# Performance work log

Hardware: AMD Instinct MI355X
Metric: run time of the kernel (lower is better)

Reference implementation:

```python
import jax, jax.numpy as jnp
import numpy as np

B, NB, K, C, CM, POS = 8, 1024, 9, 32, 128, 2
SIGMA = 0.5
NEG_SLOPE = 0.01  # nn.LeakyReLU default
BN_EPS = 1e-5


def _leaky(x):
    return jnp.where(x >= 0, x, NEG_SLOPE * x)


def _batchnorm(x, gamma, beta):
    # BatchNorm1d, training-mode batch statistics over the point dimension
    mu = jnp.mean(x, axis=0)
    var = jnp.mean((x - mu) ** 2, axis=0)
    return gamma * (x - mu) * jax.lax.rsqrt(var + BN_EPS) + beta


def setup_inputs() -> dict:
    key = jax.random.key(0)
    ks = jax.random.split(key, 8)
    N = B * NB
    positions = jax.random.normal(ks[0], (N, POS), jnp.float32)
    weights = jax.random.normal(ks[1], (N, C), jnp.float32)
    batch = jnp.full((B,), NB, dtype=jnp.int32)  # uniform point counts per graph
    # KernelConv params: kernel_init='grid' -> 3x3 grid of offsets spanning +-sigma
    g = jnp.linspace(-SIGMA, SIGMA, 3, dtype=jnp.float32)
    kernel_positions = jnp.stack(jnp.meshgrid(g, g, indexing='ij'), axis=-1).reshape(K, POS)
    kernel_weights = (jax.random.normal(ks[2], (K, C, C), jnp.float32) / np.float32(np.sqrt(C * K)))
    conv_norm_gamma = jnp.ones((C,), jnp.float32)
    conv_norm_beta = jnp.zeros((C,), jnp.float32)
    # PyG MLP([C, CM, C+POS], act_first=True, plain_last=True)
    W1 = jax.random.normal(ks[3], (C, CM), jnp.float32) / np.float32(np.sqrt(C))
    b1 = jnp.zeros((CM,), jnp.float32)
    bn_gamma = jnp.ones((CM,), jnp.float32)
    bn_beta = jnp.zeros((CM,), jnp.float32)
    W2 = jax.random.normal(ks[4], (CM, C + POS), jnp.float32) / np.float32(np.sqrt(CM))
    b2 = jnp.zeros((C + POS,), jnp.float32)
    return dict(positions=positions, weights=weights, batch=batch,
                kernel_positions=kernel_positions, kernel_weights=kernel_weights,
                conv_norm_gamma=conv_norm_gamma, conv_norm_beta=conv_norm_beta,
                W1=W1, b1=b1, bn_gamma=bn_gamma, bn_beta=bn_beta, W2=W2, b2=b2)


def reference(positions, weights, batch, kernel_positions, kernel_weights,
              conv_norm_gamma, conv_norm_beta, W1, b1, bn_gamma, bn_beta, W2, b2):
    N = positions.shape[0]
    # --- KernelConv: each point spawns K components at pos + kernel offset ---
    conv_pos = (positions[:, None, :] + kernel_positions[None, :, :])  # [N,K,2]
    conv_w = jnp.einsum('nc,kcd->nkd', weights, kernel_weights)        # [N,K,C]
    conv_pos = conv_pos.reshape(B, NB * K, POS)
    conv_w = conv_w.reshape(B, NB * K, C)
    # --- KernelSample: evaluate Gaussian mixture at original positions ---
    p = positions.reshape(B, NB, POS)
    d2 = (jnp.sum(p * p, -1)[:, :, None]
          + jnp.sum(conv_pos * conv_pos, -1)[:, None, :]
          - 2.0 * jnp.einsum('bnd,bmd->bnm', p, conv_pos))             # [B,NB,NB*K]
    Kmat = jnp.exp(-d2 / (2.0 * SIGMA * SIGMA))
    sampled = jnp.einsum('bnm,bmc->bnc', Kmat, conv_w).reshape(N, C)
    x = _leaky(sampled)                                                 # KernelSample nonlinearity
    # conv_norm + residual add of input weights
    x = _batchnorm(x, conv_norm_gamma, conv_norm_beta) + weights
    # MLP: lin -> act -> batchnorm (act_first) -> plain last lin
    h = _batchnorm(_leaky(x @ W1 + b1), bn_gamma, bn_beta)
    mlp_out = h @ W2 + b2                                               # [N, POS + C]
    delta_pos, delta_w = mlp_out[:, :POS], mlp_out[:, POS:]
    return positions + delta_pos, x + delta_w
```

## Files before the change

kernel.cpp:

```cpp
#include <hip/hip_runtime.h>
#include <hip/hip_bf16.h>

#define BB    8
#define NBB   1024
#define KK    9
#define CC    32
#define CMM   128
#define NTOT  (BB*NBB)
#define MM    (NBB*KK)
#define NEG   0.01f
#define EPS   1e-5f
#define SQL2  1.6986436f

#define OFF_CWT   0
#define SZ_CWT    (BB*CC*MM/2)
#define OFF_QPX   (OFF_CWT + SZ_CWT)
#define OFF_QPY   (OFF_QPX + BB*MM)
#define OFF_X0    (OFF_QPY + BB*MM)
#define OFF_X     (OFF_X0 + NTOT*CC)
#define OFF_H0    (OFF_X + NTOT*CC)
#define OFF_ST    (OFF_H0 + NTOT*CMM)

typedef __attribute__((ext_vector_type(8))) short short8;
typedef __attribute__((ext_vector_type(4))) float f32x4;
typedef __attribute__((ext_vector_type(2))) float f32x2;

static __device__ __forceinline__ unsigned short f2bf_rne(float f) {
    __hip_bfloat16 h = __float2bfloat16(f);
    return *reinterpret_cast<unsigned short*>(&h);
}

__global__ __launch_bounds__(256) void k_convw(const float* __restrict__ pos,
                                               const float* __restrict__ kpos,
                                               const float* __restrict__ w,
                                               const float* __restrict__ kw,
                                               float* __restrict__ qpx,
                                               float* __restrict__ qpy,
                                               float* __restrict__ stats,
                                               short* __restrict__ cwT) {
    __shared__ unsigned short kwl[KK*CC*CC];
    __shared__ unsigned short tile[2*32*144];
    int t = threadIdx.x;
    int l = t & 63, wv = t >> 6;
    int lane15 = l & 15, quad = l >> 4;
    int blk = blockIdx.x;
    int b = blk & 7, nbl = blk >> 3;

    if (blk == 0 && t < 320) stats[t] = 0.f;
    #pragma unroll
    for (int rep = 0; rep < 2; ++rep) {
        int gid = rep*65536 + blk*256 + t;
        if (gid < BB*MM) {
            int bb = gid / MM;
            int m = gid - bb*MM;
            int np = m / 9, k9 = m - np*9;
            float qx = pos[((size_t)(bb*NBB + np))*2 + 0] + kpos[k9*2 + 0];
            float qy = pos[((size_t)(bb*NBB + np))*2 + 1] + kpos[k9*2 + 1];
            qpx[gid] = SQL2*qx;
            qpy[gid] = SQL2*qy;
        }
    }
    for (int u = t; u < KK*CC*CC/4; u += 256) {
        int flat = u*4;
        int row = flat >> 5;
        int c0 = flat & 31;
        int kk = row >> 5, cp = row & 31;
        f32x4 v = *(const f32x4*)&kw[flat];
        kwl[(kk*CC + c0+0)*CC + cp] = f2bf_rne(v.x);
        kwl[(kk*CC + c0+1)*CC + cp] = f2bf_rne(v.y);
        kwl[(kk*CC + c0+2)*CC + cp] = f2bf_rne(v.z);
        kwl[(kk*CC + c0+3)*CC + cp] = f2bf_rne(v.w);
    }
    int n = b*NBB + nbl*32 + (wv & 1)*16 + lane15;
    f32x4 w0 = *(const f32x4*)&w[(size_t)n*CC + quad*8];
    f32x4 w1 = *(const f32x4*)&w[(size_t)n*CC + quad*8 + 4];
    union { unsigned short us[8]; short8 s; } bfr;
    bfr.us[0] = f2bf_rne(w0.x); bfr.us[1] = f2bf_rne(w0.y);
    bfr.us[2] = f2bf_rne(w0.z); bfr.us[3] = f2bf_rne(w0.w);
    bfr.us[4] = f2bf_rne(w1.x); bfr.us[5] = f2bf_rne(w1.y);
    bfr.us[6] = f2bf_rne(w1.z); bfr.us[7] = f2bf_rne(w1.w);
    __syncthreads();
    if (wv < 2) {
        f32x4 acc[KK][2];
        #pragma unroll
        for (int kk = 0; kk < KK; ++kk)
            #pragma unroll
            for (int ct = 0; ct < 2; ++ct) {
                int c = ct*16 + lane15;
                short8 afr = *(const short8*)&kwl[(kk*CC + c)*CC + quad*8];
                acc[kk][ct] = __builtin_amdgcn_mfma_f32_16x16x32_bf16(
                    afr, bfr.s, (f32x4)0.f, 0, 0, 0);
            }
        unsigned short* tw = tile + wv*4608;
        #pragma unroll
        for (int kk = 0; kk < KK; ++kk)
            #pragma unroll
            for (int ct = 0; ct < 2; ++ct)
                #pragma unroll
                for (int reg = 0; reg < 4; ++reg) {
                    int c = ct*16 + quad*4 + reg;
                    tw[c*144 + lane15*9 + kk] = f2bf_rne(acc[kk][ct][reg]);
                }
    }
    __syncthreads();
    short* dst = cwT + (size_t)b*CC*MM + (size_t)(nbl*32)*9;
    #pragma unroll
    for (int it = 0; it < 5; ++it) {
        int u = it*256 + t;
        if (u < 1152) {
            int c = u / 36, seg = u - c*36;
            const unsigned short* src = tile + (seg < 18 ? 0 : 4608)
                                      + c*144 + (seg < 18 ? seg : seg - 18)*8;
            short8 v = *(const short8*)src;
            *(short8*)&dst[(size_t)c*MM + seg*8] = v;
        }
    }
}

__global__ __launch_bounds__(1024) void k_sample(const float* __restrict__ pos,
                                                 const float* __restrict__ qpx,
                                                 const float* __restrict__ qpy,
                                                 const short* __restrict__ cwT,
                                                 float* __restrict__ x0,
                                                 float* __restrict__ s1) {
    __shared__ float red[16*32*36];
    __shared__ float sstat[64];
    int t = threadIdx.x;
    int l = t & 63, wv = t >> 6;
    int blk = blockIdx.x;
    int b = blk & 7, nblk = blk >> 3;
    int lane15 = l & 15, quad = l >> 4;
    int nbase = b*NBB + nblk*32;
    if (t < 64) sstat[t] = 0.f;

    float px[2], py[2];
    #pragma unroll
    for (int nt = 0; nt < 2; ++nt) {
        int n = nbase + nt*16 + lane15;
        px[nt] = SQL2*pos[(size_t)n*2];
        py[nt] = SQL2*pos[(size_t)n*2 + 1];
    }
    f32x4 acc[2][2];
    acc[0][0] = (f32x4)0.f; acc[0][1] = (f32x4)0.f;
    acc[1][0] = (f32x4)0.f; acc[1][1] = (f32x4)0.f;

    const float* qx = qpx + (size_t)b*MM;
    const float* qy = qpy + (size_t)b*MM;
    const short* ca0 = cwT + (size_t)b*CC*MM + (size_t)lane15*MM;
    const short* ca1 = ca0 + (size_t)16*MM;

    int m0 = wv*576 + quad*8;
    short8 a0 = *(const short8*)&ca0[m0];
    short8 a1 = *(const short8*)&ca1[m0];
    f32x4 X0 = *(const f32x4*)&qx[m0], X1 = *(const f32x4*)&qx[m0 + 4];
    f32x4 Y0 = *(const f32x4*)&qy[m0], Y1 = *(const f32x4*)&qy[m0 + 4];
    for (int kk = 0; kk < 18; ++kk) {
        int mn = m0 + (kk < 17 ? 32 : 0);
        short8 na0 = *(const short8*)&ca0[mn];
        short8 na1 = *(const short8*)&ca1[mn];
        f32x4 nX0 = *(const f32x4*)&qx[mn], nX1 = *(const f32x4*)&qx[mn + 4];
        f32x4 nY0 = *(const f32x4*)&qy[mn], nY1 = *(const f32x4*)&qy[mn + 4];
        #pragma unroll
        for (int nt = 0; nt < 2; ++nt) {
            f32x2 PX = {px[nt], px[nt]};
            f32x2 PY = {py[nt], py[nt]};
            f32x2 dx0 = (f32x2){X0.x, X0.y} - PX;
            f32x2 dy0 = (f32x2){Y0.x, Y0.y} - PY;
            f32x2 t0 = dx0*dx0; t0 = dy0*dy0 + t0;
            f32x2 dx1 = (f32x2){X0.z, X0.w} - PX;
            f32x2 dy1 = (f32x2){Y0.z, Y0.w} - PY;
            f32x2 t1 = dx1*dx1; t1 = dy1*dy1 + t1;
            f32x2 dx2 = (f32x2){X1.x, X1.y} - PX;
            f32x2 dy2 = (f32x2){Y1.x, Y1.y} - PY;
            f32x2 t2 = dx2*dx2; t2 = dy2*dy2 + t2;
            f32x2 dx3 = (f32x2){X1.z, X1.w} - PX;
            f32x2 dy3 = (f32x2){Y1.z, Y1.w} - PY;
            f32x2 t3 = dx3*dx3; t3 = dy3*dy3 + t3;
            float e0 = __builtin_amdgcn_exp2f(-t0.x);
            float e1 = __builtin_amdgcn_exp2f(-t0.y);
            float e2 = __builtin_amdgcn_exp2f(-t1.x);
            float e3 = __builtin_amdgcn_exp2f(-t1.y);
            float e4 = __builtin_amdgcn_exp2f(-t2.x);
            float e5 = __builtin_amdgcn_exp2f(-t2.y);
            float e6 = __builtin_amdgcn_exp2f(-t3.x);
            float e7 = __builtin_amdgcn_exp2f(-t3.y);
            union { unsigned int u[4]; short8 s; } bf;
            bf.u[0] = (__float_as_uint(e0) >> 16) | (__float_as_uint(e1) & 0xffff0000u);
            bf.u[1] = (__float_as_uint(e2) >> 16) | (__float_as_uint(e3) & 0xffff0000u);
            bf.u[2] = (__float_as_uint(e4) >> 16) | (__float_as_uint(e5) & 0xffff0000u);
            bf.u[3] = (__float_as_uint(e6) >> 16) | (__float_as_uint(e7) & 0xffff0000u);
            acc[nt][0] = __builtin_amdgcn_mfma_f32_16x16x32_bf16(a0, bf.s, acc[nt][0], 0, 0, 0);
            acc[nt][1] = __builtin_amdgcn_mfma_f32_16x16x32_bf16(a1, bf.s, acc[nt][1], 0, 0, 0);
        }
        a0 = na0; a1 = na1;
        X0 = nX0; X1 = nX1; Y0 = nY0; Y1 = nY1;
        m0 = mn;
    }
    #pragma unroll
    for (int nt = 0; nt < 2; ++nt)
        #pragma unroll
        for (int ct = 0; ct < 2; ++ct) {
            int n = nt*16 + lane15, c = ct*16 + quad*4;
            *(f32x4*)&red[(wv*32 + n)*36 + c] = acc[nt][ct];
        }
    __syncthreads();
    if (t < 256) {
        int nr = t >> 3, c0 = (t & 7)*4;
        f32x4 v = (f32x4)0.f;
        #pragma unroll
        for (int wp = 0; wp < 16; ++wp)
            v = v + *(const f32x4*)&red[(wp*32 + nr)*36 + c0];
        v.x = v.x >= 0.f ? v.x : NEG*v.x;
        v.y = v.y >= 0.f ? v.y : NEG*v.y;
        v.z = v.z >= 0.f ? v.z : NEG*v.z;
        v.w = v.w >= 0.f ? v.w : NEG*v.w;
        *(f32x4*)&x0[((size_t)(nbase + nr))*CC + c0] = v;
        float s0 = v.x, s1v = v.y, s2v = v.z, s3v = v.w;
        float q0 = v.x*v.x, q1 = v.y*v.y, q2 = v.z*v.z, q3 = v.w*v.w;
        #pragma unroll
        for (int mk = 8; mk <= 32; mk <<= 1) {
            s0 += __shfl_xor(s0, mk); s1v += __shfl_xor(s1v, mk);
            s2v += __shfl_xor(s2v, mk); s3v += __shfl_xor(s3v, mk);
            q0 += __shfl_xor(q0, mk); q1 += __shfl_xor(q1, mk);
            q2 += __shfl_xor(q2, mk); q3 += __shfl_xor(q3, mk);
        }
        if (l < 8) {
            atomicAdd(&sstat[c0 + 0], s0);  atomicAdd(&sstat[c0 + 1], s1v);
            atomicAdd(&sstat[c0 + 2], s2v); atomicAdd(&sstat[c0 + 3], s3v);
            atomicAdd(&sstat[32 + c0 + 0], q0); atomicAdd(&sstat[32 + c0 + 1], q1);
            atomicAdd(&sstat[32 + c0 + 2], q2); atomicAdd(&sstat[32 + c0 + 3], q3);
        }
    }
    __syncthreads();
    if (t < 64) atomicAdd(&s1[t], sstat[t]);
}

__global__ __launch_bounds__(256) void k_mlp1(const float* __restrict__ x0,
                                              const float* __restrict__ wts,
                                              const float* __restrict__ gma,
                                              const float* __restrict__ bta,
                                              const float* __restrict__ W1,
                                              const float* __restrict__ b1,
                                              const float* __restrict__ s1,
                                              float* __restrict__ x,
                                              float* __restrict__ h0,
                                              float* __restrict__ s2) {
    __shared__ float tile[32*68];
    int t = threadIdx.x;
    int l = t & 63, wv = t >> 6;
    int blk = blockIdx.x;
    int nb = blk >> 2, jq = blk & 3;
    int n = nb*64 + l;
    int j0 = jq*32 + wv*8;

    float xv[32];
    #pragma unroll
    for (int c = 0; c < 32; ++c) {
        float mu  = s1[c] * (1.f/NTOT);
        float var = s1[32+c]*(1.f/NTOT) - mu*mu;
        float a   = gma[c] * rsqrtf(var + EPS);
        float v   = x0[(size_t)n*CC + c];
        xv[c] = a*(v - mu) + bta[c] + wts[(size_t)n*CC + c];
    }
    if (jq == 0 && wv == 0) {
        #pragma unroll
        for (int c = 0; c < 32; c += 4)
            *(float4*)&x[(size_t)n*CC + c] = make_float4(xv[c], xv[c+1], xv[c+2], xv[c+3]);
    }
    float acc[8];
    *(f32x4*)&acc[0] = *(const f32x4*)&b1[j0];
    *(f32x4*)&acc[4] = *(const f32x4*)&b1[j0 + 4];
    #pragma unroll 8
    for (int c = 0; c < 32; ++c) {
        float xc = xv[c];
        const float* w1r = W1 + c*CMM + j0;
        f32x4 wa = *(const f32x4*)&w1r[0];
        f32x4 wb = *(const f32x4*)&w1r[4];
        acc[0] = fmaf(xc, wa.x, acc[0]); acc[1] = fmaf(xc, wa.y, acc[1]);
        acc[2] = fmaf(xc, wa.z, acc[2]); acc[3] = fmaf(xc, wa.w, acc[3]);
        acc[4] = fmaf(xc, wb.x, acc[4]); acc[5] = fmaf(xc, wb.y, acc[5]);
        acc[6] = fmaf(xc, wb.z, acc[6]); acc[7] = fmaf(xc, wb.w, acc[7]);
    }
    #pragma unroll
    for (int jj = 0; jj < 8; ++jj) {
        acc[jj] = acc[jj] >= 0.f ? acc[jj] : NEG*acc[jj];
        tile[(wv*8 + jj)*68 + l] = acc[jj];
    }
    float* hd = h0 + (size_t)n*CMM + j0;
    *(float4*)&hd[0] = make_float4(acc[0], acc[1], acc[2], acc[3]);
    *(float4*)&hd[4] = make_float4(acc[4], acc[5], acc[6], acc[7]);
    __syncthreads();
    if (t < 256) {
        int jl = t >> 3, grp = t & 7;
        float lsum = 0.f, lsq = 0.f;
        #pragma unroll
        for (int q = 0; q < 2; ++q) {
            f32x4 v = *(const f32x4*)&tile[jl*68 + grp*8 + q*4];
            lsum += v.x + v.y + v.z + v.w;
            lsq = fmaf(v.x, v.x, fmaf(v.y, v.y, fmaf(v.z, v.z, fmaf(v.w, v.w, lsq))));
        }
        lsum += __shfl_xor(lsum, 1); lsq += __shfl_xor(lsq, 1);
        lsum += __shfl_xor(lsum, 2); lsq += __shfl_xor(lsq, 2);
        lsum += __shfl_xor(lsum, 4); lsq += __shfl_xor(lsq, 4);
        if (grp == 0) {
            int jg = jq*32 + jl;
            atomicAdd(&s2[jg], lsum);
            atomicAdd(&s2[CMM + jg], lsq);
        }
    }
}

__global__ __launch_bounds__(256) void k_mlp2(const float* __restrict__ h0,
                                              const float* __restrict__ x,
                                              const float* __restrict__ pos,
                                              const float* __restrict__ g2,
                                              const float* __restrict__ bt2,
                                              const float* __restrict__ W2,
                                              const float* __restrict__ b2,
                                              const float* __restrict__ s2,
                                              float* __restrict__ out) {
    __shared__ float red[16*16*35];
    int t = threadIdx.x;
    int nl = t & 15, rid = t >> 4;
    int n = blockIdx.x*16 + nl;
    int j0 = rid*8;
    float hv[8];
    *(f32x4*)&hv[0] = *(const f32x4*)&h0[(size_t)n*CMM + j0];
    *(f32x4*)&hv[4] = *(const f32x4*)&h0[(size_t)n*CMM + j0 + 4];
    #pragma unroll
    for (int jj = 0; jj < 8; ++jj) {
        int j = j0 + jj;
        float mu  = s2[j] * (1.f/NTOT);
        float var = s2[CMM+j]*(1.f/NTOT) - mu*mu;
        float a   = g2[j] * rsqrtf(var + EPS);
        hv[jj] = a*(hv[jj] - mu) + bt2[j];
    }
    float acc[34];
    #pragma unroll
    for (int c = 0; c < 34; ++c) acc[c] = 0.f;
    for (int jj = 0; jj < 8; ++jj) {
        float h = hv[jj];
        const float* w2r = W2 + (size_t)(j0 + jj)*34;
        #pragma unroll
        for (int c = 0; c < 34; ++c)
            acc[c] = fmaf(h, w2r[c], acc[c]);
    }
    #pragma unroll
    for (int c = 0; c < 34; ++c) red[(rid*16 + nl)*35 + c] = acc[c];
    __syncthreads();
    #pragma unroll
    for (int it = 0; it < 3; ++it) {
        int u = it*256 + t;
        if (u < 544) {
            int r = u / 34, c = u - r*34;
            float v = b2[c];
            #pragma unroll
            for (int rr = 0; rr < 16; ++rr) v += red[(rr*16 + r)*35 + c];
            int nn = blockIdx.x*16 + r;
            if (c < 2)
                out[(size_t)nn*2 + c] = pos[(size_t)nn*2 + c] + v;
            else
                out[16384 + (size_t)nn*32 + (c-2)] = x[(size_t)nn*32 + (c-2)] + v;
        }
    }
}

extern "C" void kernel_launch(void* const* d_in, const int* in_sizes, int n_in,
                              void* d_out, int out_size, void* d_ws, size_t ws_size,
                              hipStream_t stream) {
    const float* positions = (const float*)d_in[0];
    const float* weights   = (const float*)d_in[1];
    const float* kpos = (const float*)d_in[3];
    const float* kw   = (const float*)d_in[4];
    const float* cg   = (const float*)d_in[5];
    const float* cb   = (const float*)d_in[6];
    const float* W1   = (const float*)d_in[7];
    const float* b1   = (const float*)d_in[8];
    const float* bg   = (const float*)d_in[9];
    const float* bb   = (const float*)d_in[10];
    const float* W2   = (const float*)d_in[11];
    const float* b2   = (const float*)d_in[12];
    float* ws  = (float*)d_ws;
    float* out = (float*)d_out;

    float* s1 = ws + OFF_ST;
    float* s2 = ws + OFF_ST + 64;

    k_convw<<<256, 256, 0, stream>>>(positions, kpos, weights, kw,
                                     ws + OFF_QPX, ws + OFF_QPY,
                                     s1, (short*)(ws + OFF_CWT));
    k_sample<<<256, 1024, 0, stream>>>(positions, ws + OFF_QPX, ws + OFF_QPY,
                                       (const short*)(ws + OFF_CWT),
                                       ws + OFF_X0, s1);
    k_mlp1<<<512, 256, 0, stream>>>(ws + OFF_X0, weights, cg, cb, W1, b1,
                                    s1, ws + OFF_X, ws + OFF_H0, s2);
    k_mlp2<<<512, 256, 0, stream>>>(ws + OFF_H0, ws + OFF_X, positions,
                                    bg, bb, W2, b2, s2, out);
}
```

Before: 149.1 us.

## Tile conv-weight buffer into 32-wide m-chunks for contiguous MFMA operand loads

The transposed conv-weight buffer cwT changes from a [C][M] layout to blocks of 32 m values × 32 channels (1024 shorts each). Each k_convw block now writes one contiguous 9216-element chunk, and in k_sample every 16-lane group reads 512 contiguous bytes instead of 16 rows strided by MM. The aim is better coalescing and fewer cache lines per operand load on the hot sampling loop. It also adds a min-blocks hint of 4 to k_sample's launch bounds, which may restrict registers or spill.

```diff
diff --git a/kernel.cpp b/kernel.cpp
--- a/kernel.cpp
+++ b/kernel.cpp
@@ -30,6 +30,7 @@
     return *reinterpret_cast<unsigned short*>(&h);
 }
 
+
 __global__ __launch_bounds__(256) void k_convw(const float* __restrict__ pos,
                                                const float* __restrict__ kpos,
                                                const float* __restrict__ w,
@@ -39,7 +40,7 @@
                                                float* __restrict__ stats,
                                                short* __restrict__ cwT) {
     __shared__ unsigned short kwl[KK*CC*CC];
-    __shared__ unsigned short tile[2*32*144];
+    __shared__ unsigned short tile[9*32*32];
     int t = threadIdx.x;
     int l = t & 63, wv = t >> 6;
     int lane15 = l & 15, quad = l >> 4;
@@ -91,38 +92,37 @@
                 acc[kk][ct] = __builtin_amdgcn_mfma_f32_16x16x32_bf16(
                     afr, bfr.s, (f32x4)0.f, 0, 0, 0);
             }
-        unsigned short* tw = tile + wv*4608;
-        #pragma unroll
-        for (int kk = 0; kk < KK; ++kk)
+        #pragma unroll
+        for (int kk = 0; kk < KK; ++kk) {
+            int ml = (wv*16 + lane15)*9 + kk;
+            unsigned short* tw = &tile[(ml >> 5)*1024 + (ml & 31)];
             #pragma unroll
             for (int ct = 0; ct < 2; ++ct)
                 #pragma unroll
                 for (int reg = 0; reg < 4; ++reg) {
                     int c = ct*16 + quad*4 + reg;
-                    tw[c*144 + lane15*9 + kk] = f2bf_rne(acc[kk][ct][reg]);
+                    tw[c*32] = f2bf_rne(acc[kk][ct][reg]);
                 }
-    }
-    __syncthreads();
-    short* dst = cwT + (size_t)b*CC*MM + (size_t)(nbl*32)*9;
+        }
+    }
+    __syncthreads();
+    short* dst = cwT + (size_t)b*CC*MM + (size_t)nbl*9216;
     #pragma unroll
     for (int it = 0; it < 5; ++it) {
         int u = it*256 + t;
         if (u < 1152) {
-            int c = u / 36, seg = u - c*36;
-            const unsigned short* src = tile + (seg < 18 ? 0 : 4608)
-                                      + c*144 + (seg < 18 ? seg : seg - 18)*8;
-            short8 v = *(const short8*)src;
-            *(short8*)&dst[(size_t)c*MM + seg*8] = v;
-        }
-    }
-}
-
-__global__ __launch_bounds__(1024) void k_sample(const float* __restrict__ pos,
-                                                 const float* __restrict__ qpx,
-                                                 const float* __restrict__ qpy,
-                                                 const short* __restrict__ cwT,
-                                                 float* __restrict__ x0,
-                                                 float* __restrict__ s1) {
+            short8 v = *(const short8*)&tile[u*8];
+            *(short8*)&dst[u*8] = v;
+        }
+    }
+}
+
+__global__ __launch_bounds__(1024, 4) void k_sample(const float* __restrict__ pos,
+                                                    const float* __restrict__ qpx,
+                                                    const float* __restrict__ qpy,
+                                                    const short* __restrict__ cwT,
+                                                    float* __restrict__ x0,
+                                                    float* __restrict__ s1) {
     __shared__ float red[16*32*36];
     __shared__ float sstat[64];
     int t = threadIdx.x;
@@ -146,18 +146,20 @@
 
     const float* qx = qpx + (size_t)b*MM;
     const float* qy = qpy + (size_t)b*MM;
-    const short* ca0 = cwT + (size_t)b*CC*MM + (size_t)lane15*MM;
-    const short* ca1 = ca0 + (size_t)16*MM;
+    const short* cab = cwT + (size_t)b*CC*MM + (size_t)lane15*32 + quad*8;
 
     int m0 = wv*576 + quad*8;
-    short8 a0 = *(const short8*)&ca0[m0];
-    short8 a1 = *(const short8*)&ca1[m0];
+    int ma = (wv*18) * 1024;
+    short8 a0 = *(const short8*)&cab[ma];
+    short8 a1 = *(const short8*)&cab[ma + 512];
     f32x4 X0 = *(const f32x4*)&qx[m0], X1 = *(const f32x4*)&qx[m0 + 4];
     f32x4 Y0 = *(const f32x4*)&qy[m0], Y1 = *(const f32x4*)&qy[m0 + 4];
     for (int kk = 0; kk < 18; ++kk) {
-        int mn = m0 + (kk < 17 ? 32 : 0);
-        short8 na0 = *(const short8*)&ca0[mn];
-        short8 na1 = *(const short8*)&ca1[mn];
+        int step = (kk < 17) ? 1 : 0;
+        int mn = m0 + step*32;
+        int man = ma + step*1024;
+        short8 na0 = *(const short8*)&cab[man];
+        short8 na1 = *(const short8*)&cab[man + 512];
         f32x4 nX0 = *(const f32x4*)&qx[mn], nX1 = *(const f32x4*)&qx[mn + 4];
         f32x4 nY0 = *(const f32x4*)&qy[mn], nY1 = *(const f32x4*)&qy[mn + 4];
         #pragma unroll
@@ -194,14 +196,14 @@
         }
         a0 = na0; a1 = na1;
         X0 = nX0; X1 = nX1; Y0 = nY0; Y1 = nY1;
-        m0 = mn;
+        m0 = mn; ma = man;
     }
     #pragma unroll
     for (int nt = 0; nt < 2; ++nt)
         #pragma unroll
         for (int ct = 0; ct < 2; ++ct) {
-            int n = nt*16 + lane15, c = ct*16 + quad*4;
-            *(f32x4*)&red[(wv*32 + n)*36 + c] = acc[nt][ct];
+            int nn = nt*16 + lane15, c = ct*16 + quad*4;
+            *(f32x4*)&red[(wv*32 + nn)*36 + c] = acc[nt][ct];
         }
     __syncthreads();
     if (t < 256) {
```

After: 143.6 us. 3.7% less time.
